# Performance work log

Hardware: AMD Instinct MI355X
Metric: run time of the kernel (lower is better)

The kernel has to match this reference:

```python
import jax, jax.numpy as jnp
import numpy as np

N = 50000      # nodes per graph
E = 800000     # directed edges per graph
D_IN, C1, C2, C3, K = 96, 64, 32, 16, 16  # K = tensor_neurons (Linear(16,16) forces 16)


def setup_inputs() -> dict:
    key = jax.random.key(0)
    ks = jax.random.split(key, 18)
    def w(k, shape, scale=0.1):
        return (jax.random.normal(k, shape, jnp.float32) * scale)
    return {
        "features_1": jax.random.normal(ks[0], (N, D_IN), jnp.float32),
        "features_2": jax.random.normal(ks[1], (N, D_IN), jnp.float32),
        "edges_1": jax.random.randint(ks[2], (2, E), 0, N),
        "edges_2": jax.random.randint(ks[3], (2, E), 0, N),
        # GCN layer params (PyG GCNConv: X @ W then normalized aggregation, then + b)
        "W1": w(ks[4], (D_IN, C1)), "b1": jnp.zeros((C1,), jnp.float32),
        "W2": w(ks[5], (C1, C2)),  "b2": jnp.zeros((C2,), jnp.float32),
        "W3": w(ks[6], (C2, C3)),  "b3": jnp.zeros((C3,), jnp.float32),
        # Attention pooling weight matrix [C3, C3]
        "Wa": w(ks[7], (C3, C3)),
        # Tensor network: bilinear tensor [C3, C3, K], block [K, 2*C3], bias [K]
        "Wt": w(ks[8], (C3, C3, K)),
        "Wb": w(ks[9], (K, 2 * C3)),
        "bt": w(ks[10], (K,)),
        # fully_connected_first Linear(16,16) and scoring Linear(16,1)
        "Wfc": w(ks[11], (K, 16)), "bfc": jnp.zeros((16,), jnp.float32),
        "Wsc": w(ks[12], (16, 1)), "bsc": jnp.zeros((1,), jnp.float32),
    }


def gcn_conv(x, src, dst, W, b):
    # PyG GCNConv with self-loops: D^-1/2 (A+I) D^-1/2 (X W) + b
    h = x @ W                                   # [N, C]
    ones = jnp.ones(src.shape[0], h.dtype)
    deg = jax.ops.segment_sum(ones, dst, num_segments=N) + 1.0   # in-degree + self loop
    dinv = jax.lax.rsqrt(deg)                   # [N]
    coef = dinv[src] * dinv[dst]                # [E]
    agg = jax.ops.segment_sum(h[src] * coef[:, None], dst, num_segments=N)
    return agg + h * (dinv * dinv)[:, None] + b  # self-loop term has norm dinv_i^2


def encode(x, edges, W1, b1, W2, b2, W3, b3):
    src, dst = edges[0], edges[1]
    x = jax.nn.relu(gcn_conv(x, src, dst, W1, b1))  # dropout is a no-op in eval mode
    x = jax.nn.relu(gcn_conv(x, src, dst, W2, b2))
    return gcn_conv(x, src, dst, W3, b3)


def attention_pool(x, Wa):
    # SimGNN AttentionModule: c = tanh(mean(x Wa)); s = sigmoid(x c); rep = x^T s
    c = jnp.tanh(jnp.mean(x @ Wa, axis=0))      # [C3]
    s = jax.nn.sigmoid(x @ c)                   # [N]
    return x.T @ s                              # [C3]


def reference(features_1, features_2, edges_1, edges_2,
              W1, b1, W2, b2, W3, b3, Wa, Wt, Wb, bt, Wfc, bfc, Wsc, bsc):
    h1 = encode(features_1, edges_1, W1, b1, W2, b2, W3, b3)
    h2 = encode(features_2, edges_2, W1, b1, W2, b2, W3, b3)
    e1 = attention_pool(h1, Wa)                 # [C3]
    e2 = attention_pool(h2, Wa)                 # [C3]
    # Tensor network scoring
    bilinear = jnp.einsum('i,ijk,j->k', e1, Wt, e2)        # [K]
    block = Wb @ jnp.concatenate([e1, e2])                 # [K]
    scores = jax.nn.relu(bilinear + block + bt)            # [K]
    scores = jnp.tanh(scores @ Wfc + bfc)                  # [16]
    score = jax.nn.sigmoid(scores @ Wsc + bsc)             # [1]
    return score
```

## Files before the change

kernel.cpp:

```cpp
#include <hip/hip_runtime.h>
#include <hip/hip_bf16.h>

#define TPB 256
#define SH 6
#define BW 64

typedef unsigned short u16;
typedef __attribute__((ext_vector_type(8))) __bf16 bf16x8;
typedef __attribute__((ext_vector_type(4))) float f32x4;

__device__ __forceinline__ u16 f_to_bf(float f) {
    unsigned u = __float_as_uint(f);
    return (u16)((u + 0x7fff + ((u >> 16) & 1)) >> 16);
}
__device__ __forceinline__ unsigned pkbf(float a, float b) {
    return (unsigned)f_to_bf(a) | ((unsigned)f_to_bf(b) << 16);
}
__device__ __forceinline__ void facc(float4& a, float4 v) {
    a.x += v.x; a.y += v.y; a.z += v.z; a.w += v.w;
}

__device__ __forceinline__ void bacc8(float* __restrict__ a, uint4 d) {
    a[0] += __uint_as_float(d.x << 16);
    a[1] += __uint_as_float(d.x & 0xffff0000u);
    a[2] += __uint_as_float(d.y << 16);
    a[3] += __uint_as_float(d.y & 0xffff0000u);
    a[4] += __uint_as_float(d.z << 16);
    a[5] += __uint_as_float(d.z & 0xffff0000u);
    a[6] += __uint_as_float(d.w << 16);
    a[7] += __uint_as_float(d.w & 0xffff0000u);
}
__device__ __forceinline__ void bdec8(uint4 d, float* __restrict__ f) {
    f[0] = __uint_as_float(d.x << 16);
    f[1] = __uint_as_float(d.x & 0xffff0000u);
    f[2] = __uint_as_float(d.y << 16);
    f[3] = __uint_as_float(d.y & 0xffff0000u);
    f[4] = __uint_as_float(d.z << 16);
    f[5] = __uint_as_float(d.z & 0xffff0000u);
    f[6] = __uint_as_float(d.w << 16);
    f[7] = __uint_as_float(d.w & 0xffff0000u);
}
__device__ __forceinline__ void red8(float* __restrict__ a, int mask, int width) {
#pragma unroll
    for (int i = 0; i < 8; i++) a[i] += __shfl_xor(a[i], mask, width);
}
__device__ __forceinline__ uint4 pack8(const float* __restrict__ o) {
    uint4 h;
    h.x = pkbf(o[0], o[1]); h.y = pkbf(o[2], o[3]);
    h.z = pkbf(o[4], o[5]); h.w = pkbf(o[6], o[7]);
    return h;
}

__device__ __forceinline__ bool swz_block(int nblk, int& g, int& bx) {
    int blk = blockIdx.x;
    int j = blk & 7;
    g = j >> 2;
    bx = (blk >> 3) * 4 + (j & 3);
    return bx < nblk;
}

template <int C>
__device__ __forceinline__ void gather_sum16(const u16* __restrict__ HW,
                                             const u16* __restrict__ col,
                                             int e, int c8, int ps, int pe,
                                             float* __restrict__ acc) {
    int p = ps;
    for (; p + 8 <= pe; p += 8) {
        int j[4];
        uint4 d[4];
#pragma unroll
        for (int r = 0; r < 4; r++) j[r] = col[p + 2 * r + e];
#pragma unroll
        for (int r = 0; r < 4; r++) d[r] = *(const uint4*)&HW[(size_t)j[r] * C + c8 * 8];
#pragma unroll
        for (int r = 0; r < 4; r++) bacc8(acc, d[r]);
    }
    for (; p + 2 <= pe; p += 2) {
        int j = col[p + e];
        bacc8(acc, *(const uint4*)&HW[(size_t)j * C + c8 * 8]);
    }
    if (p < pe && e == 0) {
        int j = col[p];
        bacc8(acc, *(const uint4*)&HW[(size_t)j * C + c8 * 8]);
    }
}


__global__ void bucket_scatter_kernel(const int* __restrict__ e0, const int* __restrict__ e1,
                                      int E, int* __restrict__ bcur,
                                      int* __restrict__ ebuf0, int* __restrict__ ebuf1,
                                      int nbuk, int cap) {
    int g = blockIdx.y;
    const int* src = g ? e1 : e0;
    const int* dst = src + E;
    int* ebuf = g ? ebuf1 : ebuf0;
    int* bu = bcur + g * 1024;
    __shared__ int hist[1024];
    for (int t = threadIdx.x; t < 1024; t += TPB) hist[t] = 0;
    __syncthreads();
    int base = blockIdx.x * 4096;
    int pk[16], bk[16], rk[16];
#pragma unroll
    for (int k = 0; k < 16; k++) {
        int e = base + k * TPB + (int)threadIdx.x;
        bk[k] = -1;
        if (e < E) {
            int s = src[e], d = dst[e];
            int b = d >> SH;
            bk[k] = b;
            pk[k] = (s << SH) | (d & (BW - 1));
            rk[k] = atomicAdd(&hist[b], 1);
        }
    }
    __syncthreads();
    for (int t = threadIdx.x; t < nbuk; t += TPB) {
        int h = hist[t];
        hist[t] = h ? atomicAdd(&bu[t], h) : 0;
    }
    __syncthreads();
#pragma unroll
    for (int k = 0; k < 16; k++)
        if (bk[k] >= 0) {
            int pos = hist[bk[k]] + rk[k];
            if (pos < cap) ebuf[(size_t)bk[k] * cap + pos] = pk[k];
        }
}

__global__ void bucket_csr_kernel(const int* __restrict__ ebuf0, const int* __restrict__ ebuf1,
                                  const int* __restrict__ bcur, int n, int cap,
                                  int* __restrict__ soff0, int* __restrict__ soff1,
                                  int* __restrict__ eoff0, int* __restrict__ eoff1,
                                  float* __restrict__ dinv0, float* __restrict__ dinv1,
                                  u16* __restrict__ col0, u16* __restrict__ col1) {
    int g = blockIdx.y;
    int b = blockIdx.x;
    const int* ebuf = g ? ebuf1 : ebuf0;
    int* soff = g ? soff1 : soff0;
    int* eoff = g ? eoff1 : eoff0;
    float* dinv = g ? dinv1 : dinv0;
    u16* col = g ? col1 : col0;
    __shared__ int h[BW], nb[BW], nrank[BW];
    int tid = threadIdx.x;
    if (tid < BW) h[tid] = 0;
    __syncthreads();
    int s = b * cap;
    int cnt = min(bcur[g * 1024 + b], cap);
    int e = s + cnt;
    for (int i = s + tid; i < e; i += TPB)
        atomicAdd(&h[ebuf[i] & (BW - 1)], 1);
    __syncthreads();
    if (tid < BW) {
        int v = h[tid];
        int x = v;
        for (int d = 1; d < BW; d <<= 1) {
            int u = __shfl_up(x, d, 64);
            if (tid >= d) x += u;
        }
        int base = s + x - v;
        nb[tid] = base;
        nrank[tid] = 0;
        int node = b * BW + tid;
        if (node < n) {
            soff[node] = base;
            eoff[node] = base + v;
            dinv[node] = rsqrtf((float)v + 1.0f);
        }
    }
    __syncthreads();
    for (int i = s + tid; i < e; i += TPB) {
        int p = ebuf[i];
        int lo = p & (BW - 1);
        int r = atomicAdd(&nrank[lo], 1);
        col[nb[lo] + r] = (u16)(p >> SH);
    }
}


template <int CIN, int COUT>
__global__ void matmul_kernel(const float* __restrict__ X0, const float* __restrict__ X1,
                              const float* __restrict__ W,
                              const float* __restrict__ dinv0, const float* __restrict__ dinv1,
                              u16* __restrict__ Y0, u16* __restrict__ Y1, int n) {
    constexpr int CINP = CIN + 8;
    constexpr int NT = COUT / 16;
    constexpr int KT = CIN / 32;
    __shared__ u16 Xs[64 * CINP];
    __shared__ u16 Wt[COUT * CINP];

    int g = blockIdx.y;
    const float* X = g ? X1 : X0;
    const float* dinv = g ? dinv1 : dinv0;
    u16* Y = g ? Y1 : Y0;
    int nb0 = blockIdx.x * 64;

    for (int i = threadIdx.x; i < 64 * (CIN / 4); i += TPB) {
        int nn = i / (CIN / 4), kc = i % (CIN / 4);
        float4 v = make_float4(0.f, 0.f, 0.f, 0.f);
        if (nb0 + nn < n) v = *(const float4*)&X[(size_t)(nb0 + nn) * CIN + 4 * kc];
        ushort4 b;
        b.x = f_to_bf(v.x); b.y = f_to_bf(v.y); b.z = f_to_bf(v.z); b.w = f_to_bf(v.w);
        *(ushort4*)&Xs[nn * CINP + 4 * kc] = b;
    }
    for (int i = threadIdx.x; i < CIN * (COUT / 4); i += TPB) {
        int k = i / (COUT / 4), nc4 = i % (COUT / 4);
        float4 v = *(const float4*)&W[(size_t)k * COUT + 4 * nc4];
        Wt[(4 * nc4 + 0) * CINP + k] = f_to_bf(v.x);
        Wt[(4 * nc4 + 1) * CINP + k] = f_to_bf(v.y);
        Wt[(4 * nc4 + 2) * CINP + k] = f_to_bf(v.z);
        Wt[(4 * nc4 + 3) * CINP + k] = f_to_bf(v.w);
    }
    __syncthreads();

    int lane = threadIdx.x & 63;
    int w = threadIdx.x >> 6;
    int m = lane & 15;
    int quad = lane >> 4;

    f32x4 acc[NT];
#pragma unroll
    for (int t = 0; t < NT; t++) acc[t] = (f32x4){0.f, 0.f, 0.f, 0.f};
#pragma unroll
    for (int kt = 0; kt < KT; kt++) {
        int k0 = kt * 32 + quad * 8;
        bf16x8 a = *(const bf16x8*)&Xs[(w * 16 + m) * CINP + k0];
#pragma unroll
        for (int t = 0; t < NT; t++) {
            bf16x8 b = *(const bf16x8*)&Wt[(t * 16 + m) * CINP + k0];
            acc[t] = __builtin_amdgcn_mfma_f32_16x16x32_bf16(a, b, acc[t], 0, 0, 0);
        }
    }
#pragma unroll
    for (int r = 0; r < 4; r++) {
        int node = nb0 + w * 16 + quad * 4 + r;
        if (node < n) {
            float d = dinv[node];
#pragma unroll
            for (int t = 0; t < NT; t++)
                Y[(size_t)node * COUT + t * 16 + m] = f_to_bf(acc[t][r] * d);
        }
    }
}


template <int C, int SPLIT, int COUT2>
__global__ __launch_bounds__(TPB, 2)
void agg_mm_kernel(const u16* __restrict__ HW0, const u16* __restrict__ HW1,
                   const int* __restrict__ soff0, const int* __restrict__ soff1,
                   const int* __restrict__ eoff0, const int* __restrict__ eoff1,
                   const u16* __restrict__ col0, const u16* __restrict__ col1,
                   const float* __restrict__ dinv0, const float* __restrict__ dinv1,
                   const float* __restrict__ bias, const float* __restrict__ W2,
                   u16* __restrict__ Y0, u16* __restrict__ Y1, int n, int nblk) {
    constexpr int CHUNKS = C / 8;
    constexpr int GRP = 2 * CHUNKS;
    constexpr int TPN = GRP * SPLIT;
    constexpr int CP = C + 8;
    constexpr int NT2 = COUT2 / 16;
    constexpr int KT2 = C / 32;
    __shared__ __align__(16) u16 HsB[16 * CP];
    __shared__ __align__(16) u16 WtB[COUT2 * CP];

    int g, bx;
    if (!swz_block(nblk, g, bx)) return;
    const u16* HW = g ? HW1 : HW0;
    const int* soff = g ? soff1 : soff0;
    const int* eoff = g ? eoff1 : eoff0;
    const u16* col = g ? col1 : col0;
    const float* dinv = g ? dinv1 : dinv0;
    u16* Y = g ? Y1 : Y0;

    for (int idx = threadIdx.x; idx < C * COUT2; idx += TPB) {
        int k = idx / COUT2, nc = idx % COUT2;
        WtB[nc * CP + k] = f_to_bf(W2[idx]);
    }

    int nl = threadIdx.x >> 4;
    int part = threadIdx.x & 15;
    int sp = part / GRP;
    int gl = part % GRP;
    int e = gl / CHUNKS;
    int c8 = gl % CHUNKS;
    int node = bx * 16 + nl;

    float acc[8], o8[8];
#pragma unroll
    for (int i = 0; i < 8; i++) { acc[i] = 0.f; o8[i] = 0.f; }

    if (node < n) {
        int s = soff[node], en = eoff[node];
        int len = en - s;
        int chunk = (len + SPLIT - 1) / SPLIT;
        int ps = s + sp * chunk;
        int pe = min(ps + chunk, en);
        gather_sum16<C>(HW, col, e, c8, ps, pe, acc);
        red8(acc, CHUNKS, TPN);
#pragma unroll
        for (int m = GRP; m < TPN; m <<= 1) red8(acc, m, TPN);
        if (part < CHUNKS) {
            float di = dinv[node];
            float sv[8];
            bdec8(*(const uint4*)&HW[(size_t)node * C + part * 8], sv);
            float4 b0 = *(const float4*)&bias[part * 8];
            float4 b1 = *(const float4*)&bias[part * 8 + 4];
            o8[0] = fmaxf(di * (acc[0] + sv[0]) + b0.x, 0.f);
            o8[1] = fmaxf(di * (acc[1] + sv[1]) + b0.y, 0.f);
            o8[2] = fmaxf(di * (acc[2] + sv[2]) + b0.z, 0.f);
            o8[3] = fmaxf(di * (acc[3] + sv[3]) + b0.w, 0.f);
            o8[4] = fmaxf(di * (acc[4] + sv[4]) + b1.x, 0.f);
            o8[5] = fmaxf(di * (acc[5] + sv[5]) + b1.y, 0.f);
            o8[6] = fmaxf(di * (acc[6] + sv[6]) + b1.z, 0.f);
            o8[7] = fmaxf(di * (acc[7] + sv[7]) + b1.w, 0.f);
        }
    }
    if (part < CHUNKS) {
        *(uint4*)&HsB[nl * CP + part * 8] = pack8(o8);
    }
    __syncthreads();

    int lane = threadIdx.x & 63;
    int w = threadIdx.x >> 6;
    if (w < NT2) {
        int m = lane & 15;
        int quad = lane >> 4;
        f32x4 ac = (f32x4){0.f, 0.f, 0.f, 0.f};
#pragma unroll
        for (int kt = 0; kt < KT2; kt++) {
            int k0 = kt * 32 + quad * 8;
            bf16x8 a = *(const bf16x8*)&HsB[m * CP + k0];
            bf16x8 b = *(const bf16x8*)&WtB[(w * 16 + m) * CP + k0];
            ac = __builtin_amdgcn_mfma_f32_16x16x32_bf16(a, b, ac, 0, 0, 0);
        }
        int base16 = bx * 16;
#pragma unroll
        for (int r = 0; r < 4; r++) {
            int onode = base16 + quad * 4 + r;
            if (onode < n)
                Y[(size_t)onode * COUT2 + w * 16 + m] = f_to_bf(ac[r] * dinv[onode]);
        }
    }
}

__global__ __launch_bounds__(TPB, 2)
void agg16_kernel(const u16* __restrict__ HW0, const u16* __restrict__ HW1,
                  const int* __restrict__ soff0, const int* __restrict__ soff1,
                  const int* __restrict__ eoff0, const int* __restrict__ eoff1,
                  const u16* __restrict__ col0, const u16* __restrict__ col1,
                  const float* __restrict__ dinv0, const float* __restrict__ dinv1,
                  const float* __restrict__ bias,
                  u16* __restrict__ out0, u16* __restrict__ out1,
                  float* __restrict__ pcol, int n, int nblk) {
    int g, bx;
    if (!swz_block(nblk, g, bx)) return;
    const u16* HW = g ? HW1 : HW0;
    const int* soff = g ? soff1 : soff0;
    const int* eoff = g ? eoff1 : eoff0;
    const u16* col = g ? col1 : col0;
    const float* dinv = g ? dinv1 : dinv0;
    u16* outp = g ? out1 : out0;

    int nl = threadIdx.x >> 4;
    int part = threadIdx.x & 15;
    int sp = part >> 2;
    int gl = part & 3;
    int e = gl >> 1;
    int c8 = gl & 1;
    int node = bx * 16 + nl;

    float acc[8], o8v[8];
#pragma unroll
    for (int i = 0; i < 8; i++) { acc[i] = 0.f; o8v[i] = 0.f; }

    if (node < n) {
        int s = soff[node], en = eoff[node];
        int len = en - s;
        int chunk = (len + 3) >> 2;
        int ps = s + sp * chunk;
        int pe = min(ps + chunk, en);
        gather_sum16<16>(HW, col, e, c8, ps, pe, acc);
        red8(acc, 2, 16);
        red8(acc, 4, 16);
        red8(acc, 8, 16);
        if (part < 2) {
            float di = dinv[node];
            float sv[8];
            bdec8(*(const uint4*)&HW[(size_t)node * 16 + part * 8], sv);
            float4 b0 = *(const float4*)&bias[part * 8];
            float4 b1 = *(const float4*)&bias[part * 8 + 4];
            o8v[0] = di * (acc[0] + sv[0]) + b0.x;
            o8v[1] = di * (acc[1] + sv[1]) + b0.y;
            o8v[2] = di * (acc[2] + sv[2]) + b0.z;
            o8v[3] = di * (acc[3] + sv[3]) + b0.w;
            o8v[4] = di * (acc[4] + sv[4]) + b1.x;
            o8v[5] = di * (acc[5] + sv[5]) + b1.y;
            o8v[6] = di * (acc[6] + sv[6]) + b1.z;
            o8v[7] = di * (acc[7] + sv[7]) + b1.w;
            *(uint4*)&outp[(size_t)node * 16 + part * 8] = pack8(o8v);
        }
    }
    __shared__ float4 sa[TPB], sb[TPB];
    bool hold = (node < n) && (part < 2);
    sa[threadIdx.x] = hold ? make_float4(o8v[0], o8v[1], o8v[2], o8v[3])
                           : make_float4(0.f, 0.f, 0.f, 0.f);
    sb[threadIdx.x] = hold ? make_float4(o8v[4], o8v[5], o8v[6], o8v[7])
                           : make_float4(0.f, 0.f, 0.f, 0.f);
    __syncthreads();
    if (threadIdx.x < 64) {
        float4 a = sa[threadIdx.x], b = sb[threadIdx.x];
        facc(a, sa[threadIdx.x + 64]);  facc(b, sb[threadIdx.x + 64]);
        facc(a, sa[threadIdx.x + 128]); facc(b, sb[threadIdx.x + 128]);
        facc(a, sa[threadIdx.x + 192]); facc(b, sb[threadIdx.x + 192]);
        sa[threadIdx.x] = a; sb[threadIdx.x] = b;
    }
    __syncthreads();
    if (threadIdx.x < 16) {
        float4 a = sa[threadIdx.x], b = sb[threadIdx.x];
        facc(a, sa[threadIdx.x + 16]); facc(b, sb[threadIdx.x + 16]);
        facc(a, sa[threadIdx.x + 32]); facc(b, sb[threadIdx.x + 32]);
        facc(a, sa[threadIdx.x + 48]); facc(b, sb[threadIdx.x + 48]);
        sa[threadIdx.x] = a; sb[threadIdx.x] = b;
    }
    __syncthreads();
    if (threadIdx.x < 2) {
        float* dst = &pcol[((size_t)g * nblk + bx) * 16 + threadIdx.x * 8];
        *(float4*)&dst[0] = sa[threadIdx.x];
        *(float4*)&dst[4] = sb[threadIdx.x];
    }
}


__global__ void cvec_kernel(const float* __restrict__ pcol, int nb16, float n_inv,
                            const float* __restrict__ Wa, float* __restrict__ cvec) {
    int g = blockIdx.x;
    const float4* p4 = (const float4*)(pcol + (size_t)g * nb16 * 16);
    __shared__ float4 sd[TPB];
    __shared__ float cs[16];
    int c4 = threadIdx.x & 3;
    int row = threadIdx.x >> 2;
    float4 acc = make_float4(0.f, 0.f, 0.f, 0.f);
    for (int r = row; r < nb16; r += 64) facc(acc, p4[(size_t)r * 4 + c4]);
    sd[threadIdx.x] = acc;
    __syncthreads();
    if (threadIdx.x < 64) {
        float4 a = sd[threadIdx.x];
        facc(a, sd[threadIdx.x + 64]);
        facc(a, sd[threadIdx.x + 128]);
        facc(a, sd[threadIdx.x + 192]);
        sd[threadIdx.x] = a;
    }
    __syncthreads();
    if (threadIdx.x < 16) {
        float4 a = sd[threadIdx.x];
        facc(a, sd[threadIdx.x + 16]);
        facc(a, sd[threadIdx.x + 32]);
        facc(a, sd[threadIdx.x + 48]);
        sd[threadIdx.x] = a;
    }
    __syncthreads();
    if (threadIdx.x < 4) {
        float4 a = sd[threadIdx.x];
        facc(a, sd[threadIdx.x + 4]);
        facc(a, sd[threadIdx.x + 8]);
        facc(a, sd[threadIdx.x + 12]);
        cs[threadIdx.x * 4 + 0] = a.x * n_inv;
        cs[threadIdx.x * 4 + 1] = a.y * n_inv;
        cs[threadIdx.x * 4 + 2] = a.z * n_inv;
        cs[threadIdx.x * 4 + 3] = a.w * n_inv;
    }
    __syncthreads();
    if (threadIdx.x < 16) {
        float acc2 = 0.f;
#pragma unroll
        for (int i = 0; i < 16; i++) acc2 += cs[i] * Wa[i * 16 + threadIdx.x];
        cvec[g * 16 + threadIdx.x] = tanhf(acc2);
    }
}


__global__ void pool_kernel(const u16* __restrict__ H0, const u16* __restrict__ H1, int n,
                            const float* __restrict__ cvec, float* __restrict__ ppool) {
    int g = blockIdx.y;
    const u16* H = g ? H1 : H0;
    int c = threadIdx.x & 15;
    float cv = cvec[g * 16 + c];
    int w = (blockIdx.x * blockDim.x + threadIdx.x) / 16;
    int stride = (gridDim.x * blockDim.x) / 16;
    float acc = 0.f;
    for (int node = w; node < n; node += stride) {
        float x = __uint_as_float((unsigned)H[(size_t)node * 16 + c] << 16);
        float p = x * cv;
        p += __shfl_xor(p, 1, 16);
        p += __shfl_xor(p, 2, 16);
        p += __shfl_xor(p, 4, 16);
        p += __shfl_xor(p, 8, 16);
        float s = 1.f / (1.f + __expf(-p));
        acc += s * x;
    }
    __shared__ float sdata[TPB];
    sdata[threadIdx.x] = acc;
    __syncthreads();
    if (threadIdx.x < 16) {
        float s = 0.f;
        for (int t = threadIdx.x; t < TPB; t += 16) s += sdata[t];
        ppool[((size_t)g * gridDim.x + blockIdx.x) * 16 + threadIdx.x] = s;
    }
}


__global__ void final_kernel(const float* __restrict__ ppool, int nbp,
                             const float* __restrict__ Wt, const float* __restrict__ Wb,
                             const float* __restrict__ bt, const float* __restrict__ Wfc,
                             const float* __restrict__ bfc, const float* __restrict__ Wsc,
                             const float* __restrict__ bsc, float* __restrict__ out) {
    __shared__ float4 sd4[TPB];
    __shared__ float rep[32], part[TPB], scores[16], tvec[16];
    int t = threadIdx.x;
    {
        const float4* p4 = (const float4*)ppool;
        int g = t >> 7;
        int r0 = (t >> 2) & 31;
        int c4 = t & 3;
        float4 acc = make_float4(0.f, 0.f, 0.f, 0.f);
        for (int r = r0; r < nbp; r += 32)
            facc(acc, p4[((size_t)g * nbp + r) * 4 + c4]);
        sd4[t] = acc;
        __syncthreads();
        for (int st = 16; st >= 1; st >>= 1) {
            if (r0 < st) facc(sd4[t], sd4[t + st * 4]);
            __syncthreads();
        }
        if (r0 == 0) {
            float4 a = sd4[t];
            rep[g * 16 + c4 * 4 + 0] = a.x;
            rep[g * 16 + c4 * 4 + 1] = a.y;
            rep[g * 16 + c4 * 4 + 2] = a.z;
            rep[g * 16 + c4 * 4 + 3] = a.w;
        }
        __syncthreads();
    }
    {
        int p = t >> 4, tt = t & 15;
        float b = 0.f;
#pragma unroll
        for (int q = 0; q < 16; q++)
            b += rep[q] * Wt[(q * 16 + p) * 16 + tt];
        part[t] = b * rep[16 + p];
    }
    __syncthreads();
    if (t < 16) {
        float bil = 0.f;
#pragma unroll
        for (int p = 0; p < 16; p++) bil += part[p * 16 + t];
        float blk = 0.f;
#pragma unroll
        for (int m = 0; m < 16; m++)
            blk += Wb[t * 32 + m] * rep[m] + Wb[t * 32 + 16 + m] * rep[16 + m];
        scores[t] = fmaxf(bil + blk + bt[t], 0.f);
    }
    __syncthreads();
    if (t < 16) {
        float acc = bfc[t];
#pragma unroll
        for (int k = 0; k < 16; k++) acc += scores[k] * Wfc[k * 16 + t];
        tvec[t] = tanhf(acc);
    }
    __syncthreads();
    if (t == 0) {
        float acc = bsc[0];
#pragma unroll
        for (int j = 0; j < 16; j++) acc += tvec[j] * Wsc[j];
        out[0] = 1.f / (1.f + __expf(-acc));
    }
}


extern "C" void kernel_launch(void* const* d_in, const int* in_sizes, int n_in,
                              void* d_out, int out_size, void* d_ws, size_t ws_size,
                              hipStream_t stream) {
    const float* X1 = (const float*)d_in[0];
    const float* X2 = (const float*)d_in[1];
    const int* edges1 = (const int*)d_in[2];
    const int* edges2 = (const int*)d_in[3];
    const float* W1 = (const float*)d_in[4];
    const float* b1 = (const float*)d_in[5];
    const float* W2 = (const float*)d_in[6];
    const float* b2 = (const float*)d_in[7];
    const float* W3 = (const float*)d_in[8];
    const float* b3 = (const float*)d_in[9];
    const float* Wa = (const float*)d_in[10];
    const float* Wt = (const float*)d_in[11];
    const float* Wb = (const float*)d_in[12];
    const float* bt = (const float*)d_in[13];
    const float* Wfc = (const float*)d_in[14];
    const float* bfc = (const float*)d_in[15];
    const float* Wsc = (const float*)d_in[16];
    const float* bsc = (const float*)d_in[17];
    float* out = (float*)d_out;

    const int N = in_sizes[0] / 96;
    const int E = in_sizes[2] / 2;
    const int NBUK = (N + BW - 1) / BW;
    int cap = ((2 * (E / NBUK)) + 255) & ~255;
    if (cap < 256) cap = 256;

    char* ws = (char*)d_ws;
    size_t o = 0;
    auto alloc = [&](size_t bytes) {
        void* p = ws + o;
        o += (bytes + 255) & ~(size_t)255;
        return p;
    };
    int* bcur = (int*)alloc((size_t)2 * 1024 * 4);
    int* soff0 = (int*)alloc((size_t)N * 4);
    int* soff1 = (int*)alloc((size_t)N * 4);
    int* eoff0 = (int*)alloc((size_t)N * 4);
    int* eoff1 = (int*)alloc((size_t)N * 4);
    u16* col0 = (u16*)alloc((size_t)NBUK * cap * 2);
    u16* col1 = (u16*)alloc((size_t)NBUK * cap * 2);
    int* ebuf0 = (int*)alloc((size_t)NBUK * cap * 4);
    int* ebuf1 = (int*)alloc((size_t)NBUK * cap * 4);
    float* dinv0 = (float*)alloc((size_t)N * 4);
    float* dinv1 = (float*)alloc((size_t)N * 4);
    u16* hwbA0 = (u16*)alloc((size_t)N * 64 * 2);
    u16* hwbA1 = (u16*)alloc((size_t)N * 64 * 2);
    u16* hwbB0 = (u16*)alloc((size_t)N * 32 * 2);
    u16* hwbB1 = (u16*)alloc((size_t)N * 32 * 2);
    u16* hwbC0 = (u16*)alloc((size_t)N * 16 * 2);
    u16* hwbC1 = (u16*)alloc((size_t)N * 16 * 2);
    u16* H30 = (u16*)alloc((size_t)N * 16 * 2);
    u16* H31 = (u16*)alloc((size_t)N * 16 * 2);

    const int gB2 = (E + 4095) / 4096;
    const int g16 = ((size_t)N * 16 + TPB - 1) / TPB;
    const int gSwz = 8 * ((g16 + 3) / 4);
    const int gMM = (N + 63) / 64;
    const int gPool = 256;

    float* pcol = (float*)alloc((size_t)2 * g16 * 16 * 4);
    float* cvecArr = (float*)alloc(32 * 4);
    float* ppool = (float*)alloc((size_t)2 * gPool * 16 * 4);

    hipMemsetAsync(bcur, 0, (size_t)2 * 1024 * 4, stream);

    bucket_scatter_kernel<<<dim3(gB2, 2), TPB, 0, stream>>>(edges1, edges2, E, bcur,
                                                            ebuf0, ebuf1, NBUK, cap);
    bucket_csr_kernel<<<dim3(NBUK, 2), TPB, 0, stream>>>(ebuf0, ebuf1, bcur, N, cap,
                                                         soff0, soff1, eoff0, eoff1,
                                                         dinv0, dinv1, col0, col1);

    matmul_kernel<96, 64><<<dim3(gMM, 2), TPB, 0, stream>>>(X1, X2, W1, dinv0, dinv1,
                                                            hwbA0, hwbA1, N);
    agg_mm_kernel<64, 1, 32><<<gSwz, TPB, 0, stream>>>(
        hwbA0, hwbA1, soff0, soff1, eoff0, eoff1, col0, col1, dinv0, dinv1, b1, W2,
        hwbB0, hwbB1, N, g16);
    agg_mm_kernel<32, 2, 16><<<gSwz, TPB, 0, stream>>>(
        hwbB0, hwbB1, soff0, soff1, eoff0, eoff1, col0, col1, dinv0, dinv1, b2, W3,
        hwbC0, hwbC1, N, g16);
    agg16_kernel<<<gSwz, TPB, 0, stream>>>(
        hwbC0, hwbC1, soff0, soff1, eoff0, eoff1, col0, col1, dinv0, dinv1, b3,
        H30, H31, pcol, N, g16);

    cvec_kernel<<<2, TPB, 0, stream>>>(pcol, g16, 1.0f / (float)N, Wa, cvecArr);
    pool_kernel<<<dim3(gPool, 2), TPB, 0, stream>>>(H30, H31, N, cvecArr, ppool);
    final_kernel<<<1, 256, 0, stream>>>(ppool, gPool, Wt, Wb, bt, Wfc, bfc, Wsc, bsc, out);
}
```

Baseline: 255.1 us.

## Aggregate first GCN layer directly from edge buckets with LDS atomics

Replaces the CSR-based first-layer aggregation with a kernel that reads the unsorted per-bucket edge lists and accumulates neighbor features into a shared-memory float tile using LDS atomic adds. The same kernel then applies bias and ReLU and runs the fused MFMA matmul by W2. This sidesteps the CSR gather layout and per-node segment handling for the widest layer, at the cost of heavy LDS atomic contention (8 atomics per 16-byte gather) and non-deterministic summation order. It assumes 64-node buckets match the BW/SH packing.

Measured after the change: 810.9 us. 3.18x slower.

```diff
diff --git a/kernel.cpp b/kernel.cpp
--- a/kernel.cpp
+++ b/kernel.cpp
@@ -237,6 +237,112 @@
 #pragma unroll
             for (int t = 0; t < NT; t++)
                 Y[(size_t)node * COUT + t * 16 + m] = f_to_bf(acc[t][r] * d);
+        }
+    }
+}
+
+
+__global__ __launch_bounds__(TPB, 2)
+void bucket_agg64_kernel(const u16* __restrict__ HW0, const u16* __restrict__ HW1,
+                         const int* __restrict__ ebuf0, const int* __restrict__ ebuf1,
+                         const int* __restrict__ bcur, int cap,
+                         const float* __restrict__ dinv0, const float* __restrict__ dinv1,
+                         const float* __restrict__ bias, const float* __restrict__ W2,
+                         u16* __restrict__ Y0, u16* __restrict__ Y1, int n, int nbuk) {
+    constexpr int C = 64, COUT2 = 32;
+    constexpr int AS = C + 4;
+    constexpr int CP = C + 8;
+    __shared__ float Hacc[64 * AS];
+    __shared__ __align__(16) u16 HsB[64 * CP];
+    __shared__ __align__(16) u16 WtB[COUT2 * CP];
+
+    int g, bx;
+    if (!swz_block(nbuk, g, bx)) return;
+    const u16* HW = g ? HW1 : HW0;
+    const int* ebuf = (g ? ebuf1 : ebuf0) + (size_t)bx * cap;
+    const float* dinv = g ? dinv1 : dinv0;
+    u16* Y = g ? Y1 : Y0;
+
+    for (int i = threadIdx.x; i < 64 * AS; i += TPB) Hacc[i] = 0.f;
+    for (int idx = threadIdx.x; idx < C * COUT2; idx += TPB) {
+        int k = idx / COUT2, nc = idx % COUT2;
+        WtB[nc * CP + k] = f_to_bf(W2[idx]);
+    }
+    __syncthreads();
+
+    int cnt = min(bcur[g * 1024 + bx], cap);
+    int slot = threadIdx.x >> 3;
+    int c = threadIdx.x & 7;
+    int base = 0;
+    for (; base + 128 <= cnt; base += 128) {
+        int p[4];
+        uint4 d[4];
+#pragma unroll
+        for (int r = 0; r < 4; r++) p[r] = ebuf[base + r * 32 + slot];
+#pragma unroll
+        for (int r = 0; r < 4; r++)
+            d[r] = *(const uint4*)&HW[(size_t)(p[r] >> SH) * C + c * 8];
+#pragma unroll
+        for (int r = 0; r < 4; r++) {
+            float t[8];
+            bdec8(d[r], t);
+            float* dst = &Hacc[(p[r] & (BW - 1)) * AS + c * 8];
+#pragma unroll
+            for (int i = 0; i < 8; i++) atomicAdd(&dst[i], t[i]);
+        }
+    }
+    for (; base < cnt; base += 32) {
+        int ei = base + slot;
+        if (ei < cnt) {
+            int p = ebuf[ei];
+            uint4 d = *(const uint4*)&HW[(size_t)(p >> SH) * C + c * 8];
+            float t[8];
+            bdec8(d, t);
+            float* dst = &Hacc[(p & (BW - 1)) * AS + c * 8];
+#pragma unroll
+            for (int i = 0; i < 8; i++) atomicAdd(&dst[i], t[i]);
+        }
+    }
+    __syncthreads();
+
+#pragma unroll
+    for (int pass = 0; pass < 2; pass++) {
+        int lo = pass * 32 + slot;
+        int node = bx * 64 + lo;
+        float o[8] = {0.f, 0.f, 0.f, 0.f, 0.f, 0.f, 0.f, 0.f};
+        if (node < n) {
+            float di = dinv[node];
+            float sv[8];
+            bdec8(*(const uint4*)&HW[(size_t)node * C + c * 8], sv);
+#pragma unroll
+            for (int i = 0; i < 8; i++)
+                o[i] = fmaxf(di * (Hacc[lo * AS + c * 8 + i] + sv[i]) + bias[c * 8 + i], 0.f);
+        }
+        *(uint4*)&HsB[lo * CP + c * 8] = pack8(o);
+    }
+    __syncthreads();
+
+    int lane = threadIdx.x & 63;
+    int w = threadIdx.x >> 6;
+    int m = lane & 15;
+    int quad = lane >> 4;
+#pragma unroll
+    for (int tt = 0; tt < 2; tt++) {
+        int tile = w + tt * 4;
+        int mrow = tile >> 1, ncol = tile & 1;
+        f32x4 ac = (f32x4){0.f, 0.f, 0.f, 0.f};
+#pragma unroll
+        for (int kt = 0; kt < 2; kt++) {
+            int k0 = kt * 32 + quad * 8;
+            bf16x8 a = *(const bf16x8*)&HsB[(mrow * 16 + m) * CP + k0];
+            bf16x8 b = *(const bf16x8*)&WtB[(ncol * 16 + m) * CP + k0];
+            ac = __builtin_amdgcn_mfma_f32_16x16x32_bf16(a, b, ac, 0, 0, 0);
+        }
+#pragma unroll
+        for (int r = 0; r < 4; r++) {
+            int onode = bx * 64 + mrow * 16 + quad * 4 + r;
+            if (onode < n)
+                Y[(size_t)onode * COUT2 + ncol * 16 + m] = f_to_bf(ac[r] * dinv[onode]);
         }
     }
 }
@@ -632,6 +738,7 @@
     const int gB2 = (E + 4095) / 4096;
     const int g16 = ((size_t)N * 16 + TPB - 1) / TPB;
     const int gSwz = 8 * ((g16 + 3) / 4);
+    const int gB1 = 8 * ((NBUK + 3) / 4);
     const int gMM = (N + 63) / 64;
     const int gPool = 256;
 
@@ -649,9 +756,9 @@
 
     matmul_kernel<96, 64><<<dim3(gMM, 2), TPB, 0, stream>>>(X1, X2, W1, dinv0, dinv1,
                                                             hwbA0, hwbA1, N);
-    agg_mm_kernel<64, 1, 32><<<gSwz, TPB, 0, stream>>>(
-        hwbA0, hwbA1, soff0, soff1, eoff0, eoff1, col0, col1, dinv0, dinv1, b1, W2,
-        hwbB0, hwbB1, N, g16);
+    bucket_agg64_kernel<<<gB1, TPB, 0, stream>>>(
+        hwbA0, hwbA1, ebuf0, ebuf1, bcur, cap, dinv0, dinv1, b1, W2,
+        hwbB0, hwbB1, N, NBUK);
     agg_mm_kernel<32, 2, 16><<<gSwz, TPB, 0, stream>>>(
         hwbB0, hwbB1, soff0, soff1, eoff0, eoff1, col0, col1, dinv0, dinv1, b2, W3,
         hwbC0, hwbC1, N, g16);
```
